# Optimization experiments

Measured on AMD Instinct MI355X. Metric: run time of the kernel, lower is better.

## Reference

```python
import jax, jax.numpy as jnp
import numpy as np

B, L, C, R = 8192, 49, 512, 128  # L = 7*7 hardcoded in module
H = W = 7


def _conv2d(x, w, b, pad):
    # x: (B, Cin, H, W), w: (Cout, Cin, k, k)
    y = jax.lax.conv_general_dilated(
        x, w, window_strides=(1, 1), padding=[(pad, pad), (pad, pad)],
        dimension_numbers=("NCHW", "OIHW", "NCHW"))
    return y + b[None, :, None, None]


def _star_relu(x, scale, bias):
    r = jnp.maximum(x, 0.0)
    return scale * (r * r) + bias


def setup_inputs() -> dict:
    key = jax.random.key(0)
    ks = jax.random.split(key, 12)
    s = 0.05
    return {
        "x": jax.random.normal(ks[0], (B, L, C), jnp.float32),
        "g_reduce_w": jax.random.normal(ks[1], (R, C), jnp.float32) * s,
        "l_reduce_w": jax.random.normal(ks[2], (R, C), jnp.float32) * s,
        "conv3_w": jax.random.normal(ks[3], (R // 2, R // 2, 3, 3), jnp.float32) * s,
        "conv3_b": jax.random.normal(ks[4], (R // 2,), jnp.float32) * s,
        "conv5_w": jax.random.normal(ks[5], (R - R // 2, R - R // 2, 5, 5), jnp.float32) * s,
        "conv5_b": jax.random.normal(ks[6], (R - R // 2,), jnp.float32) * s,
        "channel_w": jax.random.normal(ks[7], (C, R), jnp.float32) * s,
        "channel_b": jax.random.normal(ks[8], (C,), jnp.float32) * s,
        "spatial_w": jax.random.normal(ks[9], (1, 3 * R), jnp.float32) * s,
        "spatial_b": jax.random.normal(ks[10], (1,), jnp.float32) * s,
        "star_scale": jnp.ones((1,), jnp.float32),
        "star_bias": jnp.zeros((1,), jnp.float32),
    }


def reference(x, g_reduce_w, l_reduce_w, conv3_w, conv3_b, conv5_w, conv5_b,
              channel_w, channel_b, spatial_w, spatial_b, star_scale, star_bias):
    # x: (B, L, C) with L = 49 (7x7)
    # Global dual pooling over spatial (== over L)
    x_max = jnp.max(x, axis=1)   # (B, C)
    x_avg = jnp.mean(x, axis=1)  # (B, C)
    # g_reduce 1x1 conv (no bias) + StarReLU
    g1 = _star_relu(x_max @ g_reduce_w.T, star_scale, star_bias)  # (B, R)
    g2 = _star_relu(x_avg @ g_reduce_w.T, star_scale, star_bias)  # (B, R)
    # Local branch: 1x1 reduce -> HybConv2d (split 3x3 / 5x5) -> StarReLU
    x_img = x.transpose(0, 2, 1).reshape(B, C, H, W)
    x_l = jnp.einsum("bchw,rc->brhw", x_img, l_reduce_w)  # (B, R, 7, 7)
    xl1, xl2 = x_l[:, :R // 2], x_l[:, R // 2:]
    y1 = _conv2d(xl1, conv3_w, conv3_b, pad=1)
    y2 = _conv2d(xl2, conv5_w, conv5_b, pad=2)
    x_l = _star_relu(jnp.concatenate([y1, y2], axis=1), star_scale, star_bias)
    x_l = x_l.reshape(B, R, L).transpose(0, 2, 1)  # (B, L, R)
    # Channel gate: Linear(R->C) applied to each pooled branch, summed
    c_aggr = jax.nn.sigmoid((g1 @ channel_w.T + channel_b)
                            + (g2 @ channel_w.T + channel_b))  # (B, C)
    # Spatial gate: concat [x_l, g1 broadcast, g2 broadcast] -> Linear(3R->1)
    g1b = jnp.broadcast_to(g1[:, None, :], (B, L, R))
    g2b = jnp.broadcast_to(g2[:, None, :], (B, L, R))
    s_cat = jnp.concatenate([x_l, g1b, g2b], axis=-1)  # (B, L, 3R)
    s_aggr = jax.nn.sigmoid(jnp.einsum("blk,ok->blo", s_cat, spatial_w) + spatial_b)  # (B, L, 1)
    aggr = c_aggr[:, None, :] * s_aggr  # (B, L, C)
    return x * aggr
```

## Files before the change

### kernel.cpp

```cpp
#include <hip/hip_runtime.h>
#include <math.h>

#define B_ 8192
#define L_ 49
#define C_ 512
#define R_ 128

typedef short   bf16x8 __attribute__((ext_vector_type(8)));
typedef unsigned short u16x8 __attribute__((ext_vector_type(8)));
typedef float   f32x4  __attribute__((ext_vector_type(4)));

#define WS_LWF   0
#define WS_WB3F  65536
#define WS_WB5F  102400
#define WS_GWF   204800
#define WS_CWF   270336

#define SM_XB    0
#define SM_XLB   25088
#define SM_MAXB  25088
#define SM_SUMF  29184
#define SM_GA    37888
#define SM_G     38912
#define SM_CA    39936
#define SM_SPW   41984
#define SM_SP    44032
#define SM_GDOT  44288
#define SM_TOT   44304

__device__ __forceinline__ float bf2f(unsigned short u) {
    union { float f; unsigned int i; } v; v.i = ((unsigned int)u) << 16; return v.f;
}
__device__ __forceinline__ unsigned short f2bf(float f) {
    union { float f; unsigned int i; } v; v.f = f;
    unsigned int r = v.i + 0x7fffu + ((v.i >> 16) & 1u);
    return (unsigned short)(r >> 16);
}
__device__ __forceinline__ float star_relu(float x, float sc, float bi) {
    float r = fmaxf(x, 0.f);
    return sc * r * r + bi;
}
__device__ __forceinline__ float sigmoidf_(float x) {
    return 1.f / (1.f + __expf(-x));
}

__global__ void cvt_weights(const float* __restrict__ lw, const float* __restrict__ w3,
                            const float* __restrict__ w5, const float* __restrict__ gw,
                            const float* __restrict__ cw, unsigned short* __restrict__ ws)
{
    int t = blockIdx.x * blockDim.x + threadIdx.x;
    int stride = gridDim.x * blockDim.x;
    for (int i = t; i < 65536; i += stride) {
        int j = i & 7, lane = (i >> 3) & 63, ks = (i >> 9) & 15, nt = i >> 13;
        int n = nt * 16 + (lane & 15);
        int k = ks * 32 + (lane >> 4) * 8 + j;
        ws[WS_LWF + i] = f2bf(lw[n * 512 + k]);
        ws[WS_GWF + i] = f2bf(gw[n * 512 + k]);
    }
    for (int i = t; i < 65536; i += stride) {
        int j = i & 7, c = (i >> 3) & 511, r8 = i >> 12;
        ws[WS_CWF + i] = f2bf(cw[c * 128 + r8 * 8 + j]);
    }
    for (int i = t; i < 36864; i += stride) {
        int j = i & 7, lane = (i >> 3) & 63, ks = (i >> 9) & 1, f = (i >> 10) & 3, tap = i >> 12;
        int oc = f * 16 + (lane & 15);
        int ic = ks * 32 + (lane >> 4) * 8 + j;
        ws[WS_WB3F + i] = f2bf(w3[(oc * 64 + ic) * 9 + tap]);
    }
    for (int i = t; i < 102400; i += stride) {
        int j = i & 7, lane = (i >> 3) & 63, ks = (i >> 9) & 1, f = (i >> 10) & 3, tap = i >> 12;
        int oc = f * 16 + (lane & 15);
        int ic = ks * 32 + (lane >> 4) * 8 + j;
        ws[WS_WB5F + i] = f2bf(w5[(oc * 64 + ic) * 25 + tap]);
    }
}

template <int NTAP, int KD, int PAD, int COLBASE>
__device__ __forceinline__ void conv_mfma(const unsigned short* __restrict__ s_xlb,
                                          const unsigned short* __restrict__ wtbf,
                                          int m16, int kg, int ln, int f, f32x4 C[4])
{
    int lp_[4], i_[4], j_[4];
    #pragma unroll
    for (int mf = 0; mf < 4; ++mf) {
        lp_[mf] = mf * 16 + m16;
        i_[mf] = lp_[mf] / 7;
        j_[mf] = lp_[mf] % 7;
    }
    #pragma unroll
    for (int tap = 0; tap < NTAP; ++tap) {
        const int dy = tap / KD - PAD, dx = tap % KD - PAD;
        int lc[4];
        #pragma unroll
        for (int mf = 0; mf < 4; ++mf) {
            int ii = i_[mf] + dy, jj = j_[mf] + dx;
            bool v = (lp_[mf] < 49) & (ii >= 0) & (ii < 7) & (jj >= 0) & (jj < 7);
            lc[mf] = v ? (ii * 7 + jj) : 49;
        }
        #pragma unroll
        for (int ks = 0; ks < 2; ++ks) {
            bf16x8 bb = *(const bf16x8*)(wtbf + ((tap * 4 + f) * 2 + ks) * 512 + ln * 8);
            #pragma unroll
            for (int mf = 0; mf < 4; ++mf) {
                int chunk = ((COLBASE >> 3) + ks * 4 + kg) ^ (lc[mf] & 7);
                bf16x8 a = *(const bf16x8*)&s_xlb[lc[mf] * 128 + chunk * 8];
                C[mf] = __builtin_amdgcn_mfma_f32_16x16x32_bf16(a, bb, C[mf], 0, 0, 0);
            }
        }
    }
}

__global__ __launch_bounds__(512, 4)
void mafn_fused(const float* __restrict__ x,
                const float* __restrict__ b3, const float* __restrict__ b5,
                const float* __restrict__ cb, const float* __restrict__ sw,
                const float* __restrict__ sb, const float* __restrict__ ssc,
                const float* __restrict__ sbi,
                const unsigned short* __restrict__ ws,
                float* __restrict__ out)
{
    __shared__ __align__(16) unsigned char smem[SM_TOT];
    unsigned short* s_xb   = (unsigned short*)(smem + SM_XB);
    unsigned short* s_xlb  = (unsigned short*)(smem + SM_XLB);
    unsigned short* s_maxb = (unsigned short*)(smem + SM_MAXB);
    float*          s_sumf = (float*)(smem + SM_SUMF);
    unsigned short* s_ga   = (unsigned short*)(smem + SM_GA);
    float*          s_g    = (float*)(smem + SM_G);
    float*          s_ca   = (float*)(smem + SM_CA);
    float*          s_spw  = (float*)(smem + SM_SPW);
    float*          s_sp   = (float*)(smem + SM_SP);
    float*          s_gdot = (float*)(smem + SM_GDOT);

    const int b = blockIdx.x, t = threadIdx.x;
    const int wv = t >> 6, ln = t & 63;
    const int m16 = ln & 15, kg = ln >> 4;
    const float scale = ssc[0], sbias = sbi[0];

    const unsigned short* lwf  = ws + WS_LWF;
    const unsigned short* wb3f = ws + WS_WB3F;
    const unsigned short* wb5f = ws + WS_WB5F;
    const unsigned short* gwf  = ws + WS_GWF;
    const unsigned short* cwf  = ws + WS_CWF;

    f32x4 accA[4];
    f32x4 accG;
    {
        const f32x4 z = {0.f, 0.f, 0.f, 0.f};
        #pragma unroll
        for (int mf = 0; mf < 4; ++mf) accA[mf] = z;
        accG = z;
    }

    const int l0 = wv * 6;
    const int nl = (wv < 7) ? 6 : 7;

    #pragma unroll 1
    for (int h = 0; h < 2; ++h) {
        {
            const float4* x4 = (const float4*)(x + (size_t)b * (L_ * C_)) + h * 64;
            float4 mx = {-3.4e38f, -3.4e38f, -3.4e38f, -3.4e38f};
            float4 sm = {0.f, 0.f, 0.f, 0.f};
            for (int li = 0; li < nl; ++li) {
                int l = l0 + li;
                float4 v = x4[l * 128 + ln];
                mx.x = fmaxf(mx.x, v.x); mx.y = fmaxf(mx.y, v.y);
                mx.z = fmaxf(mx.z, v.z); mx.w = fmaxf(mx.w, v.w);
                sm.x += v.x; sm.y += v.y; sm.z += v.z; sm.w += v.w;
                ushort4 p;
                p.x = f2bf(v.x); p.y = f2bf(v.y); p.z = f2bf(v.z); p.w = f2bf(v.w);
                int chunk = (ln >> 1) ^ (l & 7);
                *(ushort4*)&s_xb[l * 256 + chunk * 8 + (ln & 1) * 4] = p;
            }
            ushort4 pm;
            pm.x = f2bf(mx.x); pm.y = f2bf(mx.y); pm.z = f2bf(mx.z); pm.w = f2bf(mx.w);
            *(ushort4*)&s_maxb[wv * 256 + ln * 4] = pm;
            *(float4*)&s_sumf[wv * 256 + ln * 4] = sm;
        }
        __syncthreads();

        {
            if (t < 256) {
                int c = t;
                float m = bf2f(s_maxb[c]);
                #pragma unroll
                for (int i = 1; i < 8; ++i) m = fmaxf(m, bf2f(s_maxb[i * 256 + c]));
                s_ga[c] = f2bf(m);
            } else {
                int c = t - 256;
                float s = 0.f;
                #pragma unroll
                for (int i = 0; i < 8; ++i) s += s_sumf[i * 256 + c];
                s_ga[256 + c] = f2bf(s * (1.f / 49.f));
            }
        }
        __syncthreads();

        {
            int rowA[4];
            #pragma unroll
            for (int mf = 0; mf < 4; ++mf) rowA[mf] = min(mf * 16 + m16, 48);
            #pragma unroll 2
            for (int ks = 0; ks < 8; ++ks) {
                bf16x8 bb = *(const bf16x8*)(lwf + (wv * 16 + h * 8 + ks) * 512 + ln * 8);
                #pragma unroll
                for (int mf = 0; mf < 4; ++mf) {
                    int chunk = (ks * 4 + kg) ^ (rowA[mf] & 7);
                    bf16x8 a = *(const bf16x8*)&s_xb[rowA[mf] * 256 + chunk * 8];
                    accA[mf] = __builtin_amdgcn_mfma_f32_16x16x32_bf16(a, bb, accA[mf], 0, 0, 0);
                }
            }
            const bf16x8 zz = {0,0,0,0,0,0,0,0};
            #pragma unroll 4
            for (int ks = 0; ks < 8; ++ks) {
                bf16x8 a = (m16 < 2) ? *(const bf16x8*)&s_ga[m16 * 256 + ks * 32 + kg * 8] : zz;
                bf16x8 bb = *(const bf16x8*)(gwf + (wv * 16 + h * 8 + ks) * 512 + ln * 8);
                accG = __builtin_amdgcn_mfma_f32_16x16x32_bf16(a, bb, accG, 0, 0, 0);
            }
        }
        __syncthreads();
    }

    {
        if (t < 64) ((unsigned int*)(s_xlb + 49 * 128))[t] = 0;
        const int n = wv * 16 + m16;
        #pragma unroll
        for (int mf = 0; mf < 4; ++mf) {
            #pragma unroll
            for (int rg = 0; rg < 4; ++rg) {
                int lp = mf * 16 + kg * 4 + rg;
                if (lp < 49) {
                    int idx = lp * 128 + ((((n >> 3) ^ (lp & 7)) << 3) + (n & 7));
                    s_xlb[idx] = f2bf(accA[mf][rg]);
                }
            }
        }
        if (kg == 0) {
            s_g[n]       = star_relu(accG[0], scale, sbias);
            s_g[128 + n] = star_relu(accG[1], scale, sbias);
        }
    }
    __syncthreads();

    const int f_ = wv & 3;
    const int oc_ = f_ * 16 + m16;
    {
        f32x4 C[4];
        const f32x4 z = {0.f, 0.f, 0.f, 0.f};
        #pragma unroll
        for (int mf = 0; mf < 4; ++mf) C[mf] = z;

        if (wv < 4) {
            conv_mfma<25, 5, 2, 64>(s_xlb, wb5f, m16, kg, ln, f_, C);
        } else {
            conv_mfma< 9, 3, 1,  0>(s_xlb, wb3f, m16, kg, ln, f_, C);
            const int idx = t - 256;
            #pragma unroll
            for (int half = 0; half < 2; ++half) {
                int c = idx + half * 256;
                float a0 = 0.f, a1 = 0.f;
                #pragma unroll 4
                for (int r8 = 0; r8 < 16; ++r8) {
                    u16x8 w = *(const u16x8*)(cwf + r8 * 4096 + c * 8);
                    float p = 0.f;
                    #pragma unroll
                    for (int k = 0; k < 8; ++k)
                        p += bf2f(w[k]) * (s_g[r8 * 8 + k] + s_g[128 + r8 * 8 + k]);
                    if (r8 & 1) a1 += p; else a0 += p;
                }
                s_ca[c] = sigmoidf_(a0 + a1 + 2.f * cb[c]);
            }
            if (wv == 7) {
                float p = s_g[ln] * sw[128 + ln] + s_g[128 + ln] * sw[256 + ln]
                        + s_g[ln + 64] * sw[128 + ln + 64] + s_g[128 + ln + 64] * sw[256 + ln + 64];
                #pragma unroll
                for (int off = 32; off > 0; off >>= 1) p += __shfl_xor(p, off);
                if (ln == 0) s_gdot[0] = p;
            }
        }

        const bool is5 = (wv < 4);
        const int ch = is5 ? 64 + oc_ : oc_;
        const float bias = is5 ? b5[oc_] : b3[oc_];
        const float sww = sw[ch];
        #pragma unroll
        for (int mf = 0; mf < 4; ++mf) {
            #pragma unroll
            for (int rg = 0; rg < 4; ++rg) {
                int lp = mf * 16 + kg * 4 + rg;
                float v = (lp < 49) ? star_relu(C[mf][rg] + bias, scale, sbias) * sww : 0.f;
                v += __shfl_xor(v, 1);
                v += __shfl_xor(v, 2);
                v += __shfl_xor(v, 4);
                v += __shfl_xor(v, 8);
                if (m16 == 0 && lp < 49) s_spw[wv * 64 + lp] = v;
            }
        }
    }
    __syncthreads();

    if (t < 49) {
        float s = s_gdot[0] + sb[0];
        #pragma unroll
        for (int w = 0; w < 8; ++w) s += s_spw[w * 64 + t];
        s_sp[t] = sigmoidf_(s);
    }
    __syncthreads();

    {
        const float4* x4 = (const float4*)(x + (size_t)b * (L_ * C_));
        float4* o4 = (float4*)(out + (size_t)b * (L_ * C_));
        const float4* ca4 = (const float4*)s_ca;
        for (int i = t; i < 49 * 128; i += 512) {
            int l = i >> 7, c4 = i & 127;
            float4 xv = x4[i];
            float g = s_sp[l];
            float4 cv = ca4[c4];
            float4 ov;
            ov.x = xv.x * cv.x * g;
            ov.y = xv.y * cv.y * g;
            ov.z = xv.z * cv.z * g;
            ov.w = xv.w * cv.w * g;
            o4[i] = ov;
        }
    }
}

extern "C" void kernel_launch(void* const* d_in, const int* in_sizes, int n_in,
                              void* d_out, int out_size, void* d_ws, size_t ws_size,
                              hipStream_t stream) {
    (void)in_sizes; (void)n_in; (void)ws_size; (void)out_size;
    const float* x    = (const float*)d_in[0];
    const float* g_w  = (const float*)d_in[1];
    const float* l_w  = (const float*)d_in[2];
    const float* w3   = (const float*)d_in[3];
    const float* b3   = (const float*)d_in[4];
    const float* w5   = (const float*)d_in[5];
    const float* b5   = (const float*)d_in[6];
    const float* cw   = (const float*)d_in[7];
    const float* cb   = (const float*)d_in[8];
    const float* sw   = (const float*)d_in[9];
    const float* sb   = (const float*)d_in[10];
    const float* ssc  = (const float*)d_in[11];
    const float* sbi  = (const float*)d_in[12];
    float* outp = (float*)d_out;
    unsigned short* ws = (unsigned short*)d_ws;

    cvt_weights<<<dim3(512), dim3(256), 0, stream>>>(l_w, w3, w5, g_w, cw, ws);
    mafn_fused<<<dim3(B_), dim3(512), 0, stream>>>(
        x, b3, b5, cb, sw, sb, ssc, sbi, ws, outp);
}
```

Before: 690.4 us.

## Zero-pad conv input in LDS, use MFMA for channel gate, packed bf16 converts

The reduced activations are now stored in a zero-padded 11x11 grid with a 136-element row stride. The conv taps become constant offsets, which removes per-tap bounds checks and XOR swizzle arithmetic. The channel gate matvec is rewritten as MFMA over a re-laid-out weight with pre-summed g1+g2 in bf16. Scalar bf16 rounding is replaced by the packed v_cvt_pk_bf16_f32 instruction. LDS use rises from about 44KB to about 77KB, which may reduce blocks per CU at launch_bounds(512,4), and the padded buffer must be zeroed every block.

New measurement: 708.0 us. +2.6%, slower.

```diff
diff --git a/kernel.cpp b/kernel.cpp
--- a/kernel.cpp
+++ b/kernel.cpp
@@ -17,16 +17,20 @@
 #define WS_CWF   270336
 
 #define SM_XB    0
-#define SM_XLB   25088
-#define SM_MAXB  25088
-#define SM_SUMF  29184
-#define SM_GA    37888
-#define SM_G     38912
-#define SM_CA    39936
-#define SM_SPW   41984
-#define SM_SP    44032
-#define SM_GDOT  44288
-#define SM_TOT   44304
+#define SM_XLP   25088
+#define SM_MAXB  58000
+#define SM_SUMF  62096
+#define SM_GA    70288
+#define SM_G     71312
+#define SM_HB    72336
+#define SM_CA    72592
+#define SM_SPW   74640
+#define SM_SP    76688
+#define SM_GDOT  76944
+#define SM_TOT   76960
+
+#define XLP_N    16456
+#define DBIAS    3264
 
 __device__ __forceinline__ float bf2f(unsigned short u) {
     union { float f; unsigned int i; } v; v.i = ((unsigned int)u) << 16; return v.f;
@@ -36,12 +40,21 @@
     unsigned int r = v.i + 0x7fffu + ((v.i >> 16) & 1u);
     return (unsigned short)(r >> 16);
 }
+__device__ __forceinline__ unsigned int pkbf(float a, float b) {
+    unsigned int r;
+    asm("v_cvt_pk_bf16_f32 %0, %1, %2" : "=v"(r) : "v"(a), "v"(b));
+    return r;
+}
 __device__ __forceinline__ float star_relu(float x, float sc, float bi) {
     float r = fmaxf(x, 0.f);
     return sc * r * r + bi;
 }
 __device__ __forceinline__ float sigmoidf_(float x) {
     return 1.f / (1.f + __expf(-x));
+}
+__device__ __forceinline__ int prowf(int lp) {
+    int pi = lp / 7, pj = lp - pi * 7;
+    return (pi + 2) * 11 + (pj + 2);
 }
 
 __global__ void cvt_weights(const float* __restrict__ lw, const float* __restrict__ w3,
@@ -58,8 +71,10 @@
         ws[WS_GWF + i] = f2bf(gw[n * 512 + k]);
     }
     for (int i = t; i < 65536; i += stride) {
-        int j = i & 7, c = (i >> 3) & 511, r8 = i >> 12;
-        ws[WS_CWF + i] = f2bf(cw[c * 128 + r8 * 8 + j]);
+        int j = i & 7, lane = (i >> 3) & 63, ks = (i >> 9) & 3, nf = i >> 11;
+        int c = nf * 16 + (lane & 15);
+        int k = ks * 32 + (lane >> 4) * 8 + j;
+        ws[WS_CWF + i] = f2bf(cw[c * 128 + k]);
     }
     for (int i = t; i < 36864; i += stride) {
         int j = i & 7, lane = (i >> 3) & 63, ks = (i >> 9) & 1, f = (i >> 10) & 3, tap = i >> 12;
@@ -76,34 +91,25 @@
 }
 
 template <int NTAP, int KD, int PAD, int COLBASE>
-__device__ __forceinline__ void conv_mfma(const unsigned short* __restrict__ s_xlb,
+__device__ __forceinline__ void conv_mfma(const unsigned short* __restrict__ s_xlp,
                                           const unsigned short* __restrict__ wtbf,
                                           int m16, int kg, int ln, int f, f32x4 C[4])
 {
-    int lp_[4], i_[4], j_[4];
+    int base[4];
     #pragma unroll
     for (int mf = 0; mf < 4; ++mf) {
-        lp_[mf] = mf * 16 + m16;
-        i_[mf] = lp_[mf] / 7;
-        j_[mf] = lp_[mf] % 7;
+        int lp = min(mf * 16 + m16, 48);
+        base[mf] = prowf(lp) * 136 + COLBASE + kg * 8 - DBIAS;
     }
     #pragma unroll
     for (int tap = 0; tap < NTAP; ++tap) {
-        const int dy = tap / KD - PAD, dx = tap % KD - PAD;
-        int lc[4];
-        #pragma unroll
-        for (int mf = 0; mf < 4; ++mf) {
-            int ii = i_[mf] + dy, jj = j_[mf] + dx;
-            bool v = (lp_[mf] < 49) & (ii >= 0) & (ii < 7) & (jj >= 0) & (jj < 7);
-            lc[mf] = v ? (ii * 7 + jj) : 49;
-        }
+        const int doff = ((tap / KD - PAD) * 11 + (tap % KD - PAD)) * 136 + DBIAS;
         #pragma unroll
         for (int ks = 0; ks < 2; ++ks) {
             bf16x8 bb = *(const bf16x8*)(wtbf + ((tap * 4 + f) * 2 + ks) * 512 + ln * 8);
             #pragma unroll
             for (int mf = 0; mf < 4; ++mf) {
-                int chunk = ((COLBASE >> 3) + ks * 4 + kg) ^ (lc[mf] & 7);
-                bf16x8 a = *(const bf16x8*)&s_xlb[lc[mf] * 128 + chunk * 8];
+                bf16x8 a = *(const bf16x8*)&s_xlp[base[mf] + doff + ks * 32];
                 C[mf] = __builtin_amdgcn_mfma_f32_16x16x32_bf16(a, bb, C[mf], 0, 0, 0);
             }
         }
@@ -121,11 +127,12 @@
 {
     __shared__ __align__(16) unsigned char smem[SM_TOT];
     unsigned short* s_xb   = (unsigned short*)(smem + SM_XB);
-    unsigned short* s_xlb  = (unsigned short*)(smem + SM_XLB);
+    unsigned short* s_xlp  = (unsigned short*)(smem + SM_XLP);
     unsigned short* s_maxb = (unsigned short*)(smem + SM_MAXB);
     float*          s_sumf = (float*)(smem + SM_SUMF);
     unsigned short* s_ga   = (unsigned short*)(smem + SM_GA);
     float*          s_g    = (float*)(smem + SM_G);
+    unsigned short* s_hb   = (unsigned short*)(smem + SM_HB);
     float*          s_ca   = (float*)(smem + SM_CA);
     float*          s_spw  = (float*)(smem + SM_SPW);
     float*          s_sp   = (float*)(smem + SM_SP);
@@ -150,6 +157,8 @@
         for (int mf = 0; mf < 4; ++mf) accA[mf] = z;
         accG = z;
     }
+
+    for (int i = t; i < XLP_N / 2; i += 512) ((unsigned int*)s_xlp)[i] = 0;
 
     const int l0 = wv * 6;
     const int nl = (wv < 7) ? 6 : 7;
@@ -166,14 +175,12 @@
                 mx.x = fmaxf(mx.x, v.x); mx.y = fmaxf(mx.y, v.y);
                 mx.z = fmaxf(mx.z, v.z); mx.w = fmaxf(mx.w, v.w);
                 sm.x += v.x; sm.y += v.y; sm.z += v.z; sm.w += v.w;
-                ushort4 p;
-                p.x = f2bf(v.x); p.y = f2bf(v.y); p.z = f2bf(v.z); p.w = f2bf(v.w);
+                uint2 p; p.x = pkbf(v.x, v.y); p.y = pkbf(v.z, v.w);
                 int chunk = (ln >> 1) ^ (l & 7);
-                *(ushort4*)&s_xb[l * 256 + chunk * 8 + (ln & 1) * 4] = p;
-            }
-            ushort4 pm;
-            pm.x = f2bf(mx.x); pm.y = f2bf(mx.y); pm.z = f2bf(mx.z); pm.w = f2bf(mx.w);
-            *(ushort4*)&s_maxb[wv * 256 + ln * 4] = pm;
+                *(uint2*)&s_xb[l * 256 + chunk * 8 + (ln & 1) * 4] = p;
+            }
+            uint2 pm; pm.x = pkbf(mx.x, mx.y); pm.y = pkbf(mx.z, mx.w);
+            *(uint2*)&s_maxb[wv * 256 + ln * 4] = pm;
             *(float4*)&s_sumf[wv * 256 + ln * 4] = sm;
         }
         __syncthreads();
@@ -221,22 +228,23 @@
     }
 
     {
-        if (t < 64) ((unsigned int*)(s_xlb + 49 * 128))[t] = 0;
         const int n = wv * 16 + m16;
         #pragma unroll
         for (int mf = 0; mf < 4; ++mf) {
             #pragma unroll
-            for (int rg = 0; rg < 4; ++rg) {
-                int lp = mf * 16 + kg * 4 + rg;
-                if (lp < 49) {
-                    int idx = lp * 128 + ((((n >> 3) ^ (lp & 7)) << 3) + (n & 7));
-                    s_xlb[idx] = f2bf(accA[mf][rg]);
-                }
+            for (int rp = 0; rp < 2; ++rp) {
+                unsigned int u = pkbf(accA[mf][rp * 2], accA[mf][rp * 2 + 1]);
+                int lp0 = mf * 16 + kg * 4 + rp * 2;
+                if (lp0 < 49)     s_xlp[prowf(lp0) * 136 + n]     = (unsigned short)u;
+                if (lp0 + 1 < 49) s_xlp[prowf(lp0 + 1) * 136 + n] = (unsigned short)(u >> 16);
             }
         }
         if (kg == 0) {
-            s_g[n]       = star_relu(accG[0], scale, sbias);
-            s_g[128 + n] = star_relu(accG[1], scale, sbias);
+            float g1v = star_relu(accG[0], scale, sbias);
+            float g2v = star_relu(accG[1], scale, sbias);
+            s_g[n] = g1v;
+            s_g[128 + n] = g2v;
+            s_hb[n] = f2bf(g1v + g2v);
         }
     }
     __syncthreads();
@@ -250,24 +258,30 @@
         for (int mf = 0; mf < 4; ++mf) C[mf] = z;
 
         if (wv < 4) {
-            conv_mfma<25, 5, 2, 64>(s_xlb, wb5f, m16, kg, ln, f_, C);
+            conv_mfma<25, 5, 2, 64>(s_xlp, wb5f, m16, kg, ln, f_, C);
         } else {
-            conv_mfma< 9, 3, 1,  0>(s_xlb, wb3f, m16, kg, ln, f_, C);
-            const int idx = t - 256;
-            #pragma unroll
-            for (int half = 0; half < 2; ++half) {
-                int c = idx + half * 256;
-                float a0 = 0.f, a1 = 0.f;
-                #pragma unroll 4
-                for (int r8 = 0; r8 < 16; ++r8) {
-                    u16x8 w = *(const u16x8*)(cwf + r8 * 4096 + c * 8);
-                    float p = 0.f;
-                    #pragma unroll
-                    for (int k = 0; k < 8; ++k)
-                        p += bf2f(w[k]) * (s_g[r8 * 8 + k] + s_g[128 + r8 * 8 + k]);
-                    if (r8 & 1) a1 += p; else a0 += p;
+            conv_mfma< 9, 3, 1,  0>(s_xlp, wb3f, m16, kg, ln, f_, C);
+            bf16x8 aH[4];
+            #pragma unroll
+            for (int ks = 0; ks < 4; ++ks) {
+                bf16x8 tt = {0,0,0,0,0,0,0,0};
+                if (m16 == 0) tt = *(const bf16x8*)&s_hb[ks * 32 + kg * 8];
+                aH[ks] = tt;
+            }
+            const int nf0 = (wv - 4) * 8;
+            #pragma unroll 2
+            for (int q = 0; q < 8; ++q) {
+                int nf = nf0 + q;
+                f32x4 acc = z;
+                #pragma unroll
+                for (int ks = 0; ks < 4; ++ks) {
+                    bf16x8 bb = *(const bf16x8*)(cwf + ((nf * 4 + ks) * 64 + ln) * 8);
+                    acc = __builtin_amdgcn_mfma_f32_16x16x32_bf16(aH[ks], bb, acc, 0, 0, 0);
                 }
-                s_ca[c] = sigmoidf_(a0 + a1 + 2.f * cb[c]);
+                if (kg == 0) {
+                    int c = nf * 16 + m16;
+                    s_ca[c] = sigmoidf_(acc[0] + 2.f * cb[c]);
+                }
             }
             if (wv == 7) {
                 float p = s_g[ln] * sw[128 + ln] + s_g[128 + ln] * sw[256 + ln]
```

## Split fused kernel into gate-computation and separate gate-apply elementwise kernels

Applied to the files above, without the earlier changes.

Gate computation (channel and spatial gates) now runs in its own kernel that writes the gates to workspace, and a grid-stride elementwise kernel applies them to x. The final multiply no longer sits in the tail of each heavy block, where it was tied to that block's occupancy. The cost is a second full read of x (about 822 MB) plus an extra launch and writes of the small gate arrays. The old fused path is kept as a fallback when the workspace is too small.

Result: slower. 1.347 ms (+95.2%).

```diff
diff --git a/kernel.cpp b/kernel.cpp
--- a/kernel.cpp
+++ b/kernel.cpp
@@ -15,6 +15,7 @@
 #define WS_WB5F  102400
 #define WS_GWF   204800
 #define WS_CWF   270336
+#define WS_WBYTES 671744
 
 #define SM_XB    0
 #define SM_XLB   25088
@@ -110,14 +111,15 @@
     }
 }
 
-__global__ __launch_bounds__(512, 4)
-void mafn_fused(const float* __restrict__ x,
+template <int WRITE_OUT>
+__device__ __forceinline__ void mafn_body(const float* __restrict__ x,
                 const float* __restrict__ b3, const float* __restrict__ b5,
                 const float* __restrict__ cb, const float* __restrict__ sw,
                 const float* __restrict__ sb, const float* __restrict__ ssc,
                 const float* __restrict__ sbi,
                 const unsigned short* __restrict__ ws,
-                float* __restrict__ out)
+                float* __restrict__ out,
+                float* __restrict__ ca_out, float* __restrict__ sp_out)
 {
     __shared__ __align__(16) unsigned char smem[SM_TOT];
     unsigned short* s_xb   = (unsigned short*)(smem + SM_XB);
@@ -306,7 +308,7 @@
     }
     __syncthreads();
 
-    {
+    if (WRITE_OUT) {
         const float4* x4 = (const float4*)(x + (size_t)b * (L_ * C_));
         float4* o4 = (float4*)(out + (size_t)b * (L_ * C_));
         const float4* ca4 = (const float4*)s_ca;
@@ -322,13 +324,65 @@
             ov.w = xv.w * cv.w * g;
             o4[i] = ov;
         }
+    } else {
+        if (t < 512) ca_out[(size_t)b * 512 + t] = s_ca[t];
+        if (t < 49)  sp_out[(size_t)b * 64 + t] = s_sp[t];
+    }
+}
+
+__global__ __launch_bounds__(512, 4)
+void mafn_gates(const float* __restrict__ x,
+                const float* __restrict__ b3, const float* __restrict__ b5,
+                const float* __restrict__ cb, const float* __restrict__ sw,
+                const float* __restrict__ sb, const float* __restrict__ ssc,
+                const float* __restrict__ sbi,
+                const unsigned short* __restrict__ ws,
+                float* __restrict__ ca_out, float* __restrict__ sp_out)
+{
+    mafn_body<0>(x, b3, b5, cb, sw, sb, ssc, sbi, ws, nullptr, ca_out, sp_out);
+}
+
+__global__ __launch_bounds__(512, 4)
+void mafn_fused(const float* __restrict__ x,
+                const float* __restrict__ b3, const float* __restrict__ b5,
+                const float* __restrict__ cb, const float* __restrict__ sw,
+                const float* __restrict__ sb, const float* __restrict__ ssc,
+                const float* __restrict__ sbi,
+                const unsigned short* __restrict__ ws,
+                float* __restrict__ out)
+{
+    mafn_body<1>(x, b3, b5, cb, sw, sb, ssc, sbi, ws, out, nullptr, nullptr);
+}
+
+__global__ __launch_bounds__(256)
+void apply_gates(const float* __restrict__ x,
+                 const float* __restrict__ ca, const float* __restrict__ sp,
+                 float* __restrict__ out)
+{
+    const long long total = (long long)B_ * (L_ * C_ / 4);
+    const int stride = gridDim.x * blockDim.x;
+    const float4* x4 = (const float4*)x;
+    float4* o4 = (float4*)out;
+    for (long long i = blockIdx.x * blockDim.x + threadIdx.x; i < total; i += stride) {
+        int b = (int)(i / 6272);
+        int r = (int)(i - (long long)b * 6272);
+        int l = r >> 7, c4 = r & 127;
+        float4 xv = x4[i];
+        float4 cv = ((const float4*)(ca + (size_t)b * 512))[c4];
+        float g = sp[(size_t)b * 64 + l];
+        float4 ov;
+        ov.x = xv.x * cv.x * g;
+        ov.y = xv.y * cv.y * g;
+        ov.z = xv.z * cv.z * g;
+        ov.w = xv.w * cv.w * g;
+        o4[i] = ov;
     }
 }
 
 extern "C" void kernel_launch(void* const* d_in, const int* in_sizes, int n_in,
                               void* d_out, int out_size, void* d_ws, size_t ws_size,
                               hipStream_t stream) {
-    (void)in_sizes; (void)n_in; (void)ws_size; (void)out_size;
+    (void)in_sizes; (void)n_in; (void)out_size;
     const float* x    = (const float*)d_in[0];
     const float* g_w  = (const float*)d_in[1];
     const float* l_w  = (const float*)d_in[2];
@@ -345,7 +399,18 @@
     float* outp = (float*)d_out;
     unsigned short* ws = (unsigned short*)d_ws;
 
+    const size_t needed = (size_t)WS_WBYTES + (size_t)B_ * 512 * 4 + (size_t)B_ * 64 * 4;
+
     cvt_weights<<<dim3(512), dim3(256), 0, stream>>>(l_w, w3, w5, g_w, cw, ws);
-    mafn_fused<<<dim3(B_), dim3(512), 0, stream>>>(
-        x, b3, b5, cb, sw, sb, ssc, sbi, ws, outp);
-}
+
+    if (ws_size >= needed) {
+        float* ca_out = (float*)((char*)d_ws + WS_WBYTES);
+        float* sp_out = ca_out + (size_t)B_ * 512;
+        mafn_gates<<<dim3(B_), dim3(512), 0, stream>>>(
+            x, b3, b5, cb, sw, sb, ssc, sbi, ws, ca_out, sp_out);
+        apply_gates<<<dim3(2048), dim3(256), 0, stream>>>(x, ca_out, sp_out, outp);
+    } else {
+        mafn_fused<<<dim3(B_), dim3(512), 0, stream>>>(
+            x, b3, b5, cb, sw, sb, ssc, sbi, ws, outp);
+    }
+}
```
